# Kernel tuning notes

Hardware: AMD Instinct MI355X
Metric: run time of the kernel (lower is better)

The kernel has to match this reference:

```python
import jax, jax.numpy as jnp
import numpy as np

B, N, DIN, A = 64, 64, 64, 32
DOUT = 128          # obs_output_dim == obs_act_output_dim == 128 (required by module wiring)
OA_IN = DIN + A     # obs_act_input_dim = 96


def _w(key, shape):
    fan_in = shape[-1]
    return jax.random.normal(key, shape, jnp.float32) / jnp.sqrt(jnp.float32(fan_in))


def setup_inputs() -> dict:
    key = jax.random.key(0)
    ks = jax.random.split(key, 14)
    return {
        "states": jax.random.normal(ks[0], (B, N, DIN), jnp.float32),
        "policies": jax.random.uniform(ks[1], (B, N, A), jnp.float32),
        "actions": jax.random.uniform(ks[2], (B, N, A), jnp.float32),
        # state_embed_preproc: Linear(obs_input_dim, 128) + LeakyReLU
        "W_se_pre": _w(ks[3], (128, DIN)),
        "b_se_pre": jnp.zeros((128,), jnp.float32),
        # key/query layers (shared between both attention stages in forward)
        "W_key": _w(ks[4], (DOUT, 128)),
        "W_query": _w(ks[5], (DOUT, 128)),
        # state_embed: Linear(obs_output_dim, 128) + LeakyReLU
        "W_se": _w(ks[6], (128, DOUT)),
        "b_se": jnp.zeros((128,), jnp.float32),
        # state_act_pol_embed: Linear(obs_act_input_dim, 128) + LeakyReLU
        "W_sap": _w(ks[7], (128, OA_IN)),
        "b_sap": jnp.zeros((128,), jnp.float32),
        # attention_value_layer: Linear(128, obs_act_output_dim)
        "W_av": _w(ks[8], (DOUT, 128)),
        # final value head
        "W_f1": _w(ks[9], (64, DOUT)),
        "W_f2": _w(ks[10], (1, 64)),
    }


def reference(states, policies, actions, W_se_pre, b_se_pre, W_key, W_query,
              W_se, b_se, W_sap, b_sap, W_av, W_f1, W_f2):
    lrelu = jax.nn.leaky_relu  # negative_slope=0.01, matches torch default
    d_k = W_key.shape[0]
    inv_sqrt_dk = 1.0 / jnp.sqrt(jnp.asarray(d_k, states.dtype))

    # stage 1: self-attention over agents on raw-state embeddings
    e = lrelu(states @ W_se_pre.T + b_se_pre)                       # [B,N,128]
    q1 = e @ W_query.T
    k1 = e @ W_key.T
    w_pre = jax.nn.softmax(jnp.einsum('bid,bjd->bij', q1, k1) * inv_sqrt_dk, axis=-1)
    # NB: attention_value_layer_preproc output is overwritten in the original forward;
    # the effective value is weight_preproc @ states_embed_preproc.
    av_pre = jnp.einsum('bij,bjd->bid', w_pre, e)                   # [B,N,128]

    # stage 2: self-attention weights over agents on re-embedded states
    se = lrelu(av_pre @ W_se.T + b_se)                              # [B,N,128]
    q2 = se @ W_query.T
    k2 = se @ W_key.T
    w = jax.nn.softmax(jnp.einsum('bid,bjd->bij', q2, k2) * inv_sqrt_dk, axis=-1)

    # obs_actions_policies[b,j,k] = (state_k, policy_k) if j==k else (state_k, action_k)
    obs_act = jnp.concatenate([states, actions], axis=-1)           # [B,N,OA_IN]
    obs_pol = jnp.concatenate([states, policies], axis=-1)
    n = states.shape[1]
    eye = jnp.eye(n, dtype=states.dtype)[None, :, :, None]          # [1,N,N,1]
    oap = eye * obs_pol[:, None, :, :] + (1.0 - eye) * obs_act[:, None, :, :]  # [B,N,N,OA_IN]

    emb = lrelu(oap @ W_sap.T + b_sap)                              # [B,N,N,128]
    av = emb @ W_av.T                                               # [B,N,N,DOUT]

    # fused form of repeat->weight->sum: node[b,i,j,d] = sum_k w[b,i,k] * av[b,j,k,d]
    node = jnp.einsum('bik,bjkd->bijd', w, av)                      # [B,N,N,DOUT]

    value = lrelu(node @ W_f1.T) @ W_f2.T                           # [B,N,N,1]
    return value, w_pre, w
```

## Files before the change

kernel.cpp:

```cpp
#include <hip/hip_runtime.h>

#define DEVFN __device__ __forceinline__

constexpr int BNN = 64 * 64 * 64;
constexpr float SCALE = 0.08838834764831845f;
constexpr float NSLOPE = 0.01f;

constexpr int OFF_WPRET = 0;
constexpr int OFF_WQT   = 8192;
constexpr int OFF_M     = 24576;
constexpr int OFF_WSET  = 40960;
constexpr int OFF_WSAPT = 57344;
constexpr int OFF_WAVT  = 69632;
constexpr int OFF_WF1T  = 86016;
constexpr int OFF_E     = 98304;
constexpr int OFF_Q     = 622592;
constexpr int OFF_ET    = 1146880;
constexpr int OFF_SET   = 1671168;
constexpr int OFF_HA    = 2195456;
constexpr int OFF_HD    = 2719744;


DEVFN void st128(int tid, const float* __restrict__ src, float* __restrict__ Bs, int rows) {
  const int n4 = rows * 32;
  for (int idx = tid; idx < n4; idx += 512) {
    const int r = idx >> 5, c = idx & 31;
    *reinterpret_cast<float4*>(&Bs[r * 132 + c * 4]) =
        *reinterpret_cast<const float4*>(&src[r * 128 + c * 4]);
  }
}

DEVFN void st64x(int tid, const float* __restrict__ src, float* __restrict__ Bs) {
  for (int idx = tid; idx < 1024; idx += 512) {
    const int r = idx >> 4, c = idx & 15;
    *reinterpret_cast<float4*>(&Bs[r * 68 + c * 4]) =
        *reinterpret_cast<const float4*>(&src[r * 64 + c * 4]);
  }
}

DEVFN void wrT(int tid, const float* __restrict__ S, float* __restrict__ dst, int rq) {
  const int fr = tid >> 2, a4 = tid & 3;
  float t[4];
#pragma unroll
  for (int i = 0; i < 4; ++i) t[i] = S[(a4 * 4 + i) * 132 + fr];
  float4 v; v.x = t[0]; v.y = t[1]; v.z = t[2]; v.w = t[3];
  *reinterpret_cast<float4*>(&dst[fr * 64 + rq * 16 + a4 * 4]) = v;
}


DEVFN void g1(int tid, const float* __restrict__ A, int lda,
              const float* __restrict__ Bs, int K, float (&acc)[4]) {
  const int c0 = (tid & 31) * 4, rg = tid >> 5;
#pragma unroll 8
  for (int k = 0; k < K; ++k) {
    const float4 bv = *reinterpret_cast<const float4*>(&Bs[k * 132 + c0]);
    const float a = A[rg * lda + k];
    acc[0] += a * bv.x; acc[1] += a * bv.y; acc[2] += a * bv.z; acc[3] += a * bv.w;
  }
}

DEVFN void g2A(int tid, const float* __restrict__ A0, const float* __restrict__ A1,
               int lda, const float* __restrict__ Bs, int K,
               float (&a0)[4], float (&a1)[4]) {
  const int c0 = (tid & 31) * 4, rg = tid >> 5;
#pragma unroll 4
  for (int k = 0; k < K; ++k) {
    const float4 bv = *reinterpret_cast<const float4*>(&Bs[k * 132 + c0]);
    const float x = A0[rg * lda + k];
    const float y = A1[rg * lda + k];
    a0[0] += x * bv.x; a0[1] += x * bv.y; a0[2] += x * bv.z; a0[3] += x * bv.w;
    a1[0] += y * bv.x; a1[1] += y * bv.y; a1[2] += y * bv.z; a1[3] += y * bv.w;
  }
}

DEVFN void gH(int tid, const float* __restrict__ A, int lda,
              const float* __restrict__ Bs, int K, float (&acc)[2]) {
  const int c0 = (tid & 31) * 2, rg = tid >> 5;
#pragma unroll 8
  for (int k = 0; k < K; ++k) {
    const float2 bv = *reinterpret_cast<const float2*>(&Bs[k * 68 + c0]);
    const float a = A[rg * lda + k];
    acc[0] += a * bv.x; acc[1] += a * bv.y;
  }
}

DEVFN void gH2(int tid, const float* __restrict__ A0, const float* __restrict__ A1,
               int lda, const float* __restrict__ Bs, int K,
               float (&a0)[2], float (&a1)[2]) {
  const int c0 = (tid & 31) * 2, rg = tid >> 5;
#pragma unroll 4
  for (int k = 0; k < K; ++k) {
    const float2 bv = *reinterpret_cast<const float2*>(&Bs[k * 68 + c0]);
    const float x = A0[rg * lda + k];
    const float y = A1[rg * lda + k];
    a0[0] += x * bv.x; a0[1] += x * bv.y;
    a1[0] += y * bv.x; a1[1] += y * bv.y;
  }
}

template<bool ACT, bool HASB>
DEVFN void epi(int tid, const float (&acc)[4], float* __restrict__ O, int ldo,
               const float* __restrict__ bias) {
  const int c0 = (tid & 31) * 4, rg = tid >> 5;
  float t[4];
#pragma unroll
  for (int i = 0; i < 4; ++i) {
    float x = acc[i];
    if constexpr (HASB) x += bias[c0 + i];
    if constexpr (ACT) x = (x > 0.f) ? x : NSLOPE * x;
    t[i] = x;
  }
  float4 v; v.x = t[0]; v.y = t[1]; v.z = t[2]; v.w = t[3];
  *reinterpret_cast<float4*>(&O[rg * ldo + c0]) = v;
}


DEVFN void score_half(int tid, const float* __restrict__ Qs, int hoff,
                      const float* __restrict__ Ks, float (&acc)[2]) {
  const int j = tid & 63, iw = tid >> 6;
#pragma unroll 2
  for (int kt = 0; kt < 64; kt += 8) {
    float qv[2][8];
#pragma unroll
    for (int r = 0; r < 2; ++r) {
      *reinterpret_cast<float4*>(&qv[r][0]) =
          *reinterpret_cast<const float4*>(&Qs[(iw * 2 + r) * 132 + hoff + kt]);
      *reinterpret_cast<float4*>(&qv[r][4]) =
          *reinterpret_cast<const float4*>(&Qs[(iw * 2 + r) * 132 + hoff + kt + 4]);
    }
#pragma unroll
    for (int kk = 0; kk < 8; ++kk) {
      const float kv = Ks[(kt + kk) * 68 + j];
      acc[0] += qv[0][kk] * kv;
      acc[1] += qv[1][kk] * kv;
    }
  }
}

DEVFN void softmax_write(int tid, float (&acc)[2], float* __restrict__ Wp,
                         float* __restrict__ gout) {
  const int j = tid & 63, iw = tid >> 6;
#pragma unroll
  for (int r = 0; r < 2; ++r) {
    float v = acc[r] * SCALE;
    float m = v;
#pragma unroll
    for (int off = 32; off > 0; off >>= 1) m = fmaxf(m, __shfl_xor(m, off, 64));
    const float p = __expf(v - m);
    float s = p;
#pragma unroll
    for (int off = 32; off > 0; off >>= 1) s += __shfl_xor(s, off, 64);
    const float w = p / s;
    Wp[(iw * 2 + r) * 68 + j] = w;
    gout[(iw * 2 + r) * 64 + j] = w;
  }
}


__global__ void transpose_all(const float* __restrict__ Wpre, const float* __restrict__ Wq,
                              const float* __restrict__ Wse, const float* __restrict__ Wsap,
                              const float* __restrict__ Wav, const float* __restrict__ Wf1,
                              float* __restrict__ ws) {
  const int m = blockIdx.y;
  const float* src; int Cout, K, off;
  switch (m) {
    case 0: src = Wpre; Cout = 128; K = 64;  off = OFF_WPRET; break;
    case 1: src = Wq;   Cout = 128; K = 128; off = OFF_WQT;   break;
    case 2: src = Wse;  Cout = 128; K = 128; off = OFF_WSET;  break;
    case 3: src = Wsap; Cout = 128; K = 96;  off = OFF_WSAPT; break;
    case 4: src = Wav;  Cout = 128; K = 128; off = OFF_WAVT;  break;
    default: src = Wf1; Cout = 64;  K = 128; off = OFF_WF1T;  break;
  }
  const int idx = blockIdx.x * 256 + threadIdx.x;
  if (idx < Cout * K) {
    const int c = idx / K, k = idx - c * K;
    ws[off + k * Cout + c] = src[idx];
  }
}

__global__ __launch_bounds__(512) void make_M(const float* __restrict__ Wkey,
                                              float* __restrict__ ws) {
  __shared__ float As[16 * 132];
  __shared__ float Bs[64 * 132];
  const int tid = threadIdx.x;
  const int r0 = blockIdx.x * 16;
  {
    const int r = tid >> 5, c = tid & 31;
    *reinterpret_cast<float4*>(&As[r * 132 + c * 4]) =
        *reinterpret_cast<const float4*>(&ws[OFF_WQT + (r0 + r) * 128 + c * 4]);
  }
  const int c0 = (tid & 31) * 4, rg = tid >> 5;
  float acc[4] = {};
  for (int h = 0; h < 2; ++h) {
    __syncthreads();
    st128(tid, Wkey + h * 8192, Bs, 64);
    __syncthreads();
#pragma unroll 8
    for (int k = 0; k < 64; ++k) {
      const float4 bv = *reinterpret_cast<const float4*>(&Bs[k * 132 + c0]);
      const float a = As[rg * 132 + h * 64 + k];
      acc[0] += a * bv.x; acc[1] += a * bv.y; acc[2] += a * bv.z; acc[3] += a * bv.w;
    }
  }
  float4 v; v.x = acc[0]; v.y = acc[1]; v.z = acc[2]; v.w = acc[3];
  *reinterpret_cast<float4*>(&ws[OFF_M + (r0 + rg) * 128 + c0]) = v;
}

__global__ __launch_bounds__(512) void P1(const float* __restrict__ states,
                                          const float* __restrict__ policies,
                                          const float* __restrict__ actions,
                                          const float* __restrict__ b_sap,
                                          const float* __restrict__ b_se_pre,
                                          float* __restrict__ ws) {
  __shared__ float S[16 * 68];
  __shared__ float Aa[16 * 36], Ap[16 * 36];
  __shared__ float Ea[16 * 132];
  __shared__ float Ep[16 * 132], Dd[16 * 132], Er[16 * 132];
  __shared__ float Bs[64 * 132];
  const int tid = threadIdx.x;
  const int wid = ((blockIdx.x & 7) << 5) | (blockIdx.x >> 3);
  const int b = wid >> 2, rq = wid & 3;
  const int r0g = b * 64 + rq * 16;

  for (int idx = tid; idx < 1024; idx += 512) {
    const int r = idx >> 6, c = idx & 63;
    S[r * 68 + c] = states[(r0g + r) * 64 + c];
  }
  {
    const int r = tid >> 5, c = tid & 31;
    Aa[r * 36 + c] = actions[(r0g + r) * 32 + c];
    Ap[r * 36 + c] = policies[(r0g + r) * 32 + c];
  }
  st128(tid, ws + OFF_WSAPT, Bs, 64);
  __syncthreads();
  float cm[4] = {};
  g1(tid, S, 68, Bs, 64, cm);
  __syncthreads();
  st128(tid, ws + OFF_WSAPT + 8192, Bs, 32);
  __syncthreads();
  float aa[4] = {cm[0], cm[1], cm[2], cm[3]};
  float ap[4] = {cm[0], cm[1], cm[2], cm[3]};
  g2A(tid, Aa, Ap, 36, Bs, 32, aa, ap);
  epi<true, true>(tid, aa, Ea, 132, b_sap);
  epi<true, true>(tid, ap, Ep, 132, b_sap);
  __syncthreads();
  for (int idx = tid; idx < 2048; idx += 512) {
    const int r = idx >> 7, c = idx & 127;
    Ep[r * 132 + c] -= Ea[r * 132 + c];
  }
  __syncthreads();
  st128(tid, ws + OFF_WAVT, Bs, 64);
  __syncthreads();
  float av[4] = {}, dl[4] = {};
  g2A(tid, Ea, Ep, 132, Bs, 64, av, dl);
  __syncthreads();
  st128(tid, ws + OFF_WAVT + 8192, Bs, 64);
  __syncthreads();
  g2A(tid, Ea + 64, Ep + 64, 132, Bs, 64, av, dl);
  __syncthreads();
  epi<false, false>(tid, av, Ea, 132, nullptr);
  epi<false, false>(tid, dl, Dd, 132, nullptr);
  __syncthreads();
  st64x(tid, ws + OFF_WF1T, Bs);
  __syncthreads();
  float ah[2] = {}, aha[2] = {};
  gH2(tid, Dd, Ea, 132, Bs, 64, ah, aha);
  __syncthreads();
  st64x(tid, ws + OFF_WF1T + 4096, Bs);
  __syncthreads();
  gH2(tid, Dd + 64, Ea + 64, 132, Bs, 64, ah, aha);
  {
    const int c0 = (tid & 31) * 2, rg = tid >> 5;
    float2 vh; vh.x = ah[0]; vh.y = ah[1];
    float2 va; va.x = aha[0]; va.y = aha[1];
    *reinterpret_cast<float2*>(&ws[OFF_HD + (r0g + rg) * 64 + c0]) = vh;
    *reinterpret_cast<float2*>(&ws[OFF_HA + (r0g + rg) * 64 + c0]) = va;
  }
  __syncthreads();
  st128(tid, ws + OFF_WPRET, Bs, 64);
  __syncthreads();
  {
    float ae[4] = {};
    g1(tid, S, 68, Bs, 64, ae);
    const int c0 = (tid & 31) * 4, rg = tid >> 5;
    float t[4];
#pragma unroll
    for (int i = 0; i < 4; ++i) {
      float x = ae[i] + b_se_pre[c0 + i];
      t[i] = (x > 0.f) ? x : NSLOPE * x;
    }
    float4 v; v.x = t[0]; v.y = t[1]; v.z = t[2]; v.w = t[3];
    *reinterpret_cast<float4*>(&Er[rg * 132 + c0]) = v;
    *reinterpret_cast<float4*>(&ws[OFF_E + (r0g + rg) * 128 + c0]) = v;
  }
  __syncthreads();
  wrT(tid, Er, ws + OFF_ET + b * 8192, rq);
  st128(tid, ws + OFF_M, Bs, 64);
  __syncthreads();
  float af[4] = {};
  g1(tid, Er, 132, Bs, 64, af);
  __syncthreads();
  st128(tid, ws + OFF_M + 8192, Bs, 64);
  __syncthreads();
  g1(tid, Er + 64, 132, Bs, 64, af);
  epi<false, false>(tid, af, ws + OFF_Q + r0g * 128, 128, nullptr);
}

__global__ __launch_bounds__(512) void P3(const float* __restrict__ b_se,
                                          float* __restrict__ ws,
                                          float* __restrict__ out) {
  __shared__ float Qs[16 * 132];
  __shared__ float Bs[64 * 132];
  __shared__ float Wp[16 * 68], AV[16 * 132], SEr[16 * 132];
  const int tid = threadIdx.x;
  const int wid = ((blockIdx.x & 7) << 5) | (blockIdx.x >> 3);
  const int b = wid >> 2, rq = wid & 3;
  const int r0g = b * 64 + rq * 16;

  {
    const int r = tid >> 5, c = tid & 31;
    *reinterpret_cast<float4*>(&Qs[r * 132 + c * 4]) =
        *reinterpret_cast<const float4*>(&ws[OFF_Q + (r0g + r) * 128 + c * 4]);
  }
  st64x(tid, ws + OFF_ET + b * 8192, Bs);
  __syncthreads();
  float sc[2] = {};
  score_half(tid, Qs, 0, Bs, sc);
  __syncthreads();
  st64x(tid, ws + OFF_ET + b * 8192 + 4096, Bs);
  __syncthreads();
  score_half(tid, Qs, 64, Bs, sc);
  softmax_write(tid, sc, Wp, out + BNN + b * 4096 + rq * 1024);
  __syncthreads();
  st128(tid, ws + OFF_E + b * 8192, Bs, 64);
  __syncthreads();
  {
    float a[4] = {};
    g1(tid, Wp, 68, Bs, 64, a);
    epi<false, false>(tid, a, AV, 132, nullptr);
  }
  __syncthreads();
  st128(tid, ws + OFF_WSET, Bs, 64);
  __syncthreads();
  float as[4] = {};
  g1(tid, AV, 132, Bs, 64, as);
  __syncthreads();
  st128(tid, ws + OFF_WSET + 8192, Bs, 64);
  __syncthreads();
  g1(tid, AV + 64, 132, Bs, 64, as);
  {
    const int c0 = (tid & 31) * 4, rg = tid >> 5;
    float t[4];
#pragma unroll
    for (int i = 0; i < 4; ++i) {
      float x = as[i] + b_se[c0 + i];
      t[i] = (x > 0.f) ? x : NSLOPE * x;
    }
    float4 v; v.x = t[0]; v.y = t[1]; v.z = t[2]; v.w = t[3];
    *reinterpret_cast<float4*>(&SEr[rg * 132 + c0]) = v;
  }
  __syncthreads();
  wrT(tid, SEr, ws + OFF_SET + b * 8192, rq);
  st128(tid, ws + OFF_M, Bs, 64);
  __syncthreads();
  float af[4] = {};
  g1(tid, SEr, 132, Bs, 64, af);
  __syncthreads();
  st128(tid, ws + OFF_M + 8192, Bs, 64);
  __syncthreads();
  g1(tid, SEr + 64, 132, Bs, 64, af);
  epi<false, false>(tid, af, ws + OFF_Q + r0g * 128, 128, nullptr);
}

__global__ __launch_bounds__(512) void P4(const float* __restrict__ Wf2g,
                                          float* __restrict__ ws,
                                          float* __restrict__ out) {
  __shared__ float Qs[16 * 132];
  __shared__ float Bs[64 * 132];
  __shared__ float Wp[16 * 68], Hb[16 * 66];
  __shared__ float Hd[64 * 69];
  __shared__ float Wf2s[64];
  const int tid = threadIdx.x;
  const int wid = ((blockIdx.x & 7) << 5) | (blockIdx.x >> 3);
  const int b = wid >> 2, rq = wid & 3;
  const int r0g = b * 64 + rq * 16;

  for (int idx = tid; idx < 4096; idx += 512)
    Hd[(idx >> 6) * 69 + (idx & 63)] = ws[OFF_HD + b * 4096 + idx];
  if (tid < 64) Wf2s[tid] = Wf2g[tid];
  {
    const int r = tid >> 5, c = tid & 31;
    *reinterpret_cast<float4*>(&Qs[r * 132 + c * 4]) =
        *reinterpret_cast<const float4*>(&ws[OFF_Q + (r0g + r) * 128 + c * 4]);
  }
  st64x(tid, ws + OFF_SET + b * 8192, Bs);
  __syncthreads();
  float sc[2] = {};
  score_half(tid, Qs, 0, Bs, sc);
  __syncthreads();
  st64x(tid, ws + OFF_SET + b * 8192 + 4096, Bs);
  __syncthreads();
  score_half(tid, Qs, 64, Bs, sc);
  softmax_write(tid, sc, Wp, out + 2 * BNN + b * 4096 + rq * 1024);
  __syncthreads();
  st64x(tid, ws + OFF_HA + b * 4096, Bs);
  __syncthreads();
  float ah[2] = {};
  gH(tid, Wp, 68, Bs, 64, ah);
  {
    const int c0 = (tid & 31) * 2, rg = tid >> 5;
    float2 v; v.x = ah[0]; v.y = ah[1];
    *reinterpret_cast<float2*>(&Hb[rg * 66 + c0]) = v;
  }
  __syncthreads();
  const int j = tid & 63, iw = tid >> 6;
  float wv[2], a2[2] = {0.f, 0.f};
#pragma unroll
  for (int r = 0; r < 2; ++r) wv[r] = Wp[(iw * 2 + r) * 68 + j];
  for (int f = 0; f < 64; ++f) {
    const float hdv = Hd[j * 69 + f];
    const float wf = Wf2s[f];
#pragma unroll
    for (int r = 0; r < 2; ++r) {
      float t = Hb[(iw * 2 + r) * 66 + f] + wv[r] * hdv;
      t = (t > 0.f) ? t : NSLOPE * t;
      a2[r] += t * wf;
    }
  }
#pragma unroll
  for (int r = 0; r < 2; ++r)
    out[(r0g + iw * 2 + r) * 64 + j] = a2[r];
}

extern "C" void kernel_launch(void* const* d_in, const int* in_sizes, int n_in,
                              void* d_out, int out_size, void* d_ws, size_t ws_size,
                              hipStream_t stream) {
  const float* states   = (const float*)d_in[0];
  const float* policies = (const float*)d_in[1];
  const float* actions  = (const float*)d_in[2];
  const float* W_se_pre = (const float*)d_in[3];
  const float* b_se_pre = (const float*)d_in[4];
  const float* W_key    = (const float*)d_in[5];
  const float* W_query  = (const float*)d_in[6];
  const float* W_se     = (const float*)d_in[7];
  const float* b_se     = (const float*)d_in[8];
  const float* W_sap    = (const float*)d_in[9];
  const float* b_sap    = (const float*)d_in[10];
  const float* W_av     = (const float*)d_in[11];
  const float* W_f1     = (const float*)d_in[12];
  const float* W_f2     = (const float*)d_in[13];
  float* out = (float*)d_out;
  float* ws  = (float*)d_ws;

  transpose_all<<<dim3(64, 6), dim3(256), 0, stream>>>(
      W_se_pre, W_query, W_se, W_sap, W_av, W_f1, ws);
  make_M<<<dim3(8), dim3(512), 0, stream>>>(W_key, ws);
  P1<<<dim3(256), dim3(512), 0, stream>>>(states, policies, actions, b_sap, b_se_pre, ws);
  P3<<<dim3(256), dim3(512), 0, stream>>>(b_se, ws, out);
  P4<<<dim3(256), dim3(512), 0, stream>>>(W_f2, ws, out);
}
```

Before: 64.59 us.

## Fuse all stages into one persistent kernel with grid-wide barriers

Replaces the five separate launches (weight transpose, M precompute, P1, P3, P4) with a single 256-block kernel. Stages are separated by atomic-counter grid barriers, and a memset resets the counters. Per-block Q tiles now stay in shared memory across stages instead of round-tripping through global memory, and the score loops load the full 128-deep K tile at once. This cuts launch overhead and global traffic, but relies on all 256 blocks being co-resident and adds spin-wait barrier costs plus a memset launch.

Result: slower. 110.8 us (+71.5%).

```diff
diff --git a/kernel.cpp b/kernel.cpp
--- a/kernel.cpp
+++ b/kernel.cpp
@@ -7,18 +7,27 @@
 constexpr float NSLOPE = 0.01f;
 
 constexpr int OFF_WPRET = 0;
-constexpr int OFF_WQT   = 8192;
+constexpr int OFF_CNT   = 8192;
 constexpr int OFF_M     = 24576;
 constexpr int OFF_WSET  = 40960;
 constexpr int OFF_WSAPT = 57344;
 constexpr int OFF_WAVT  = 69632;
 constexpr int OFF_WF1T  = 86016;
 constexpr int OFF_E     = 98304;
-constexpr int OFF_Q     = 622592;
 constexpr int OFF_ET    = 1146880;
 constexpr int OFF_SET   = 1671168;
 constexpr int OFF_HA    = 2195456;
 constexpr int OFF_HD    = 2719744;
+
+constexpr int R_WP = 0;
+constexpr int R_AA = 1088;
+constexpr int R_AP = 1664;
+constexpr int R_QS = 2240;
+constexpr int R_EP = 4352;
+constexpr int R_DD = 6464;
+constexpr int R_ER = 8576;
+constexpr int R_BS = 10880;
+constexpr int LDS_TOT = 19584;
 
 
 DEVFN void st128(int tid, const float* __restrict__ src, float* __restrict__ Bs, int rows) {
@@ -30,8 +39,9 @@
   }
 }
 
-DEVFN void st64x(int tid, const float* __restrict__ src, float* __restrict__ Bs) {
-  for (int idx = tid; idx < 1024; idx += 512) {
+DEVFN void st64r(int tid, const float* __restrict__ src, float* __restrict__ Bs, int rows) {
+  const int n4 = rows * 16;
+  for (int idx = tid; idx < n4; idx += 512) {
     const int r = idx >> 4, c = idx & 15;
     *reinterpret_cast<float4*>(&Bs[r * 68 + c * 4]) =
         *reinterpret_cast<const float4*>(&src[r * 64 + c * 4]);
@@ -115,18 +125,18 @@
 }
 
 
-DEVFN void score_half(int tid, const float* __restrict__ Qs, int hoff,
+DEVFN void score_full(int tid, const float* __restrict__ Qs,
                       const float* __restrict__ Ks, float (&acc)[2]) {
   const int j = tid & 63, iw = tid >> 6;
 #pragma unroll 2
-  for (int kt = 0; kt < 64; kt += 8) {
+  for (int kt = 0; kt < 128; kt += 8) {
     float qv[2][8];
 #pragma unroll
     for (int r = 0; r < 2; ++r) {
       *reinterpret_cast<float4*>(&qv[r][0]) =
-          *reinterpret_cast<const float4*>(&Qs[(iw * 2 + r) * 132 + hoff + kt]);
+          *reinterpret_cast<const float4*>(&Qs[(iw * 2 + r) * 132 + kt]);
       *reinterpret_cast<float4*>(&qv[r][4]) =
-          *reinterpret_cast<const float4*>(&Qs[(iw * 2 + r) * 132 + hoff + kt + 4]);
+          *reinterpret_cast<const float4*>(&Qs[(iw * 2 + r) * 132 + kt + 4]);
     }
 #pragma unroll
     for (int kk = 0; kk < 8; ++kk) {
@@ -157,279 +167,274 @@
 }
 
 
-__global__ void transpose_all(const float* __restrict__ Wpre, const float* __restrict__ Wq,
-                              const float* __restrict__ Wse, const float* __restrict__ Wsap,
-                              const float* __restrict__ Wav, const float* __restrict__ Wf1,
-                              float* __restrict__ ws) {
-  const int m = blockIdx.y;
-  const float* src; int Cout, K, off;
-  switch (m) {
-    case 0: src = Wpre; Cout = 128; K = 64;  off = OFF_WPRET; break;
-    case 1: src = Wq;   Cout = 128; K = 128; off = OFF_WQT;   break;
-    case 2: src = Wse;  Cout = 128; K = 128; off = OFF_WSET;  break;
-    case 3: src = Wsap; Cout = 128; K = 96;  off = OFF_WSAPT; break;
-    case 4: src = Wav;  Cout = 128; K = 128; off = OFF_WAVT;  break;
-    default: src = Wf1; Cout = 64;  K = 128; off = OFF_WF1T;  break;
-  }
-  const int idx = blockIdx.x * 256 + threadIdx.x;
-  if (idx < Cout * K) {
-    const int c = idx / K, k = idx - c * K;
-    ws[off + k * Cout + c] = src[idx];
-  }
-}
-
-__global__ __launch_bounds__(512) void make_M(const float* __restrict__ Wkey,
-                                              float* __restrict__ ws) {
-  __shared__ float As[16 * 132];
-  __shared__ float Bs[64 * 132];
+DEVFN void gridbar(unsigned* __restrict__ cnt, int tid) {
+  __syncthreads();
+  if (tid == 0) {
+    __threadfence();
+    atomicAdd(cnt, 1u);
+    while (atomicAdd(cnt, 0u) < 256u) { __builtin_amdgcn_s_sleep(2); }
+    __threadfence();
+  }
+  __syncthreads();
+}
+
+
+__global__ __launch_bounds__(512) void FUSED(
+    const float* __restrict__ states, const float* __restrict__ policies,
+    const float* __restrict__ actions, const float* __restrict__ Wpre,
+    const float* __restrict__ bpre, const float* __restrict__ Wkey,
+    const float* __restrict__ Wq, const float* __restrict__ Wse,
+    const float* __restrict__ bse, const float* __restrict__ Wsap,
+    const float* __restrict__ bsap, const float* __restrict__ Wav,
+    const float* __restrict__ Wf1, const float* __restrict__ Wf2,
+    float* __restrict__ ws, float* __restrict__ out) {
+  __shared__ float L[LDS_TOT];
   const int tid = threadIdx.x;
-  const int r0 = blockIdx.x * 16;
-  {
-    const int r = tid >> 5, c = tid & 31;
-    *reinterpret_cast<float4*>(&As[r * 132 + c * 4]) =
-        *reinterpret_cast<const float4*>(&ws[OFF_WQT + (r0 + r) * 128 + c * 4]);
-  }
-  const int c0 = (tid & 31) * 4, rg = tid >> 5;
-  float acc[4] = {};
-  for (int h = 0; h < 2; ++h) {
-    __syncthreads();
-    st128(tid, Wkey + h * 8192, Bs, 64);
-    __syncthreads();
-#pragma unroll 8
-    for (int k = 0; k < 64; ++k) {
-      const float4 bv = *reinterpret_cast<const float4*>(&Bs[k * 132 + c0]);
-      const float a = As[rg * 132 + h * 64 + k];
-      acc[0] += a * bv.x; acc[1] += a * bv.y; acc[2] += a * bv.z; acc[3] += a * bv.w;
-    }
-  }
-  float4 v; v.x = acc[0]; v.y = acc[1]; v.z = acc[2]; v.w = acc[3];
-  *reinterpret_cast<float4*>(&ws[OFF_M + (r0 + rg) * 128 + c0]) = v;
-}
-
-__global__ __launch_bounds__(512) void P1(const float* __restrict__ states,
-                                          const float* __restrict__ policies,
-                                          const float* __restrict__ actions,
-                                          const float* __restrict__ b_sap,
-                                          const float* __restrict__ b_se_pre,
-                                          float* __restrict__ ws) {
-  __shared__ float S[16 * 68];
-  __shared__ float Aa[16 * 36], Ap[16 * 36];
-  __shared__ float Ea[16 * 132];
-  __shared__ float Ep[16 * 132], Dd[16 * 132], Er[16 * 132];
-  __shared__ float Bs[64 * 132];
-  const int tid = threadIdx.x;
-  const int wid = ((blockIdx.x & 7) << 5) | (blockIdx.x >> 3);
+  const int bid = blockIdx.x;
+  const int wid = ((bid & 7) << 5) | (bid >> 3);
   const int b = wid >> 2, rq = wid & 3;
   const int r0g = b * 64 + rq * 16;
-
-  for (int idx = tid; idx < 1024; idx += 512) {
-    const int r = idx >> 6, c = idx & 63;
-    S[r * 68 + c] = states[(r0g + r) * 64 + c];
-  }
+  unsigned* cnt = (unsigned*)(ws + OFF_CNT);
+
   {
-    const int r = tid >> 5, c = tid & 31;
-    Aa[r * 36 + c] = actions[(r0g + r) * 32 + c];
-    Ap[r * 36 + c] = policies[(r0g + r) * 32 + c];
-  }
-  st128(tid, ws + OFF_WSAPT, Bs, 64);
-  __syncthreads();
-  float cm[4] = {};
-  g1(tid, S, 68, Bs, 64, cm);
-  __syncthreads();
-  st128(tid, ws + OFF_WSAPT + 8192, Bs, 32);
-  __syncthreads();
-  float aa[4] = {cm[0], cm[1], cm[2], cm[3]};
-  float ap[4] = {cm[0], cm[1], cm[2], cm[3]};
-  g2A(tid, Aa, Ap, 36, Bs, 32, aa, ap);
-  epi<true, true>(tid, aa, Ea, 132, b_sap);
-  epi<true, true>(tid, ap, Ep, 132, b_sap);
-  __syncthreads();
-  for (int idx = tid; idx < 2048; idx += 512) {
-    const int r = idx >> 7, c = idx & 127;
-    Ep[r * 132 + c] -= Ea[r * 132 + c];
-  }
-  __syncthreads();
-  st128(tid, ws + OFF_WAVT, Bs, 64);
-  __syncthreads();
-  float av[4] = {}, dl[4] = {};
-  g2A(tid, Ea, Ep, 132, Bs, 64, av, dl);
-  __syncthreads();
-  st128(tid, ws + OFF_WAVT + 8192, Bs, 64);
-  __syncthreads();
-  g2A(tid, Ea + 64, Ep + 64, 132, Bs, 64, av, dl);
-  __syncthreads();
-  epi<false, false>(tid, av, Ea, 132, nullptr);
-  epi<false, false>(tid, dl, Dd, 132, nullptr);
-  __syncthreads();
-  st64x(tid, ws + OFF_WF1T, Bs);
-  __syncthreads();
-  float ah[2] = {}, aha[2] = {};
-  gH2(tid, Dd, Ea, 132, Bs, 64, ah, aha);
-  __syncthreads();
-  st64x(tid, ws + OFF_WF1T + 4096, Bs);
-  __syncthreads();
-  gH2(tid, Dd + 64, Ea + 64, 132, Bs, 64, ah, aha);
+    const int gt = bid * 512 + tid;
+    if (gt < 8192) {
+      const int c = gt >> 6, k = gt & 63;
+      ws[OFF_WPRET + k * 128 + c] = Wpre[gt];
+    } else if (gt < 24576) {
+      const int i = gt - 8192, c = i >> 7, k = i & 127;
+      ws[OFF_WSET + k * 128 + c] = Wse[i];
+    } else if (gt < 36864) {
+      const int i = gt - 24576, c = i / 96, k = i - c * 96;
+      ws[OFF_WSAPT + k * 128 + c] = Wsap[i];
+    } else if (gt < 53248) {
+      const int i = gt - 36864, c = i >> 7, k = i & 127;
+      ws[OFF_WAVT + k * 128 + c] = Wav[i];
+    } else if (gt < 61440) {
+      const int i = gt - 53248, c = i >> 7, k = i & 127;
+      ws[OFF_WF1T + k * 64 + c] = Wf1[i];
+    }
+  }
+  if (bid < 8) {
+    const int r0 = bid * 16;
+    float* As = L + R_QS;
+    float* Bs = L + R_BS;
+    for (int idx = tid; idx < 2048; idx += 512) {
+      const int r = idx & 15, o = idx >> 4;
+      As[r * 132 + o] = Wq[o * 128 + r0 + r];
+    }
+    const int c0 = (tid & 31) * 4, rg = tid >> 5;
+    float acc[4] = {};
+    for (int h = 0; h < 2; ++h) {
+      __syncthreads();
+      st128(tid, Wkey + h * 8192, Bs, 64);
+      __syncthreads();
+#pragma unroll 8
+      for (int k = 0; k < 64; ++k) {
+        const float4 bv = *reinterpret_cast<const float4*>(&Bs[k * 132 + c0]);
+        const float a = As[rg * 132 + h * 64 + k];
+        acc[0] += a * bv.x; acc[1] += a * bv.y; acc[2] += a * bv.z; acc[3] += a * bv.w;
+      }
+    }
+    float4 v; v.x = acc[0]; v.y = acc[1]; v.z = acc[2]; v.w = acc[3];
+    *reinterpret_cast<float4*>(&ws[OFF_M + (r0 + rg) * 128 + c0]) = v;
+  }
+  gridbar(cnt + 0, tid);
+
   {
-    const int c0 = (tid & 31) * 2, rg = tid >> 5;
-    float2 vh; vh.x = ah[0]; vh.y = ah[1];
-    float2 va; va.x = aha[0]; va.y = aha[1];
-    *reinterpret_cast<float2*>(&ws[OFF_HD + (r0g + rg) * 64 + c0]) = vh;
-    *reinterpret_cast<float2*>(&ws[OFF_HA + (r0g + rg) * 64 + c0]) = va;
-  }
-  __syncthreads();
-  st128(tid, ws + OFF_WPRET, Bs, 64);
-  __syncthreads();
+    float* S  = L + R_WP;
+    float* Aa = L + R_AA;
+    float* Ap = L + R_AP;
+    float* Ea = L + R_QS;
+    float* Ep = L + R_EP;
+    float* Dd = L + R_DD;
+    float* Er = L + R_ER;
+    float* Bs = L + R_BS;
+
+    for (int idx = tid; idx < 1024; idx += 512) {
+      const int r = idx >> 6, c = idx & 63;
+      S[r * 68 + c] = states[(r0g + r) * 64 + c];
+    }
+    {
+      const int r = tid >> 5, c = tid & 31;
+      Aa[r * 36 + c] = actions[(r0g + r) * 32 + c];
+      Ap[r * 36 + c] = policies[(r0g + r) * 32 + c];
+    }
+    st128(tid, ws + OFF_WSAPT, Bs, 64);
+    __syncthreads();
+    float cm[4] = {};
+    g1(tid, S, 68, Bs, 64, cm);
+    __syncthreads();
+    st128(tid, ws + OFF_WSAPT + 8192, Bs, 32);
+    __syncthreads();
+    float aa[4] = {cm[0], cm[1], cm[2], cm[3]};
+    float ap[4] = {cm[0], cm[1], cm[2], cm[3]};
+    g2A(tid, Aa, Ap, 36, Bs, 32, aa, ap);
+    epi<true, true>(tid, aa, Ea, 132, bsap);
+    epi<true, true>(tid, ap, Ep, 132, bsap);
+    __syncthreads();
+    for (int idx = tid; idx < 2048; idx += 512) {
+      const int r = idx >> 7, c = idx & 127;
+      Ep[r * 132 + c] -= Ea[r * 132 + c];
+    }
+    __syncthreads();
+    st128(tid, ws + OFF_WAVT, Bs, 64);
+    __syncthreads();
+    float av[4] = {}, dl[4] = {};
+    g2A(tid, Ea, Ep, 132, Bs, 64, av, dl);
+    __syncthreads();
+    st128(tid, ws + OFF_WAVT + 8192, Bs, 64);
+    __syncthreads();
+    g2A(tid, Ea + 64, Ep + 64, 132, Bs, 64, av, dl);
+    __syncthreads();
+    epi<false, false>(tid, av, Ea, 132, nullptr);
+    epi<false, false>(tid, dl, Dd, 132, nullptr);
+    __syncthreads();
+    st64r(tid, ws + OFF_WF1T, Bs, 64);
+    __syncthreads();
+    float ah[2] = {}, aha[2] = {};
+    gH2(tid, Dd, Ea, 132, Bs, 64, ah, aha);
+    __syncthreads();
+    st64r(tid, ws + OFF_WF1T + 4096, Bs, 64);
+    __syncthreads();
+    gH2(tid, Dd + 64, Ea + 64, 132, Bs, 64, ah, aha);
+    {
+      const int c0 = (tid & 31) * 2, rg = tid >> 5;
+      float2 vh; vh.x = ah[0]; vh.y = ah[1];
+      float2 va; va.x = aha[0]; va.y = aha[1];
+      *reinterpret_cast<float2*>(&ws[OFF_HD + (r0g + rg) * 64 + c0]) = vh;
+      *reinterpret_cast<float2*>(&ws[OFF_HA + (r0g + rg) * 64 + c0]) = va;
+    }
+    __syncthreads();
+    st128(tid, ws + OFF_WPRET, Bs, 64);
+    __syncthreads();
+    {
+      float ae[4] = {};
+      g1(tid, S, 68, Bs, 64, ae);
+      const int c0 = (tid & 31) * 4, rg = tid >> 5;
+      float t[4];
+#pragma unroll
+      for (int i = 0; i < 4; ++i) {
+        float x = ae[i] + bpre[c0 + i];
+        t[i] = (x > 0.f) ? x : NSLOPE * x;
+      }
+      float4 v; v.x = t[0]; v.y = t[1]; v.z = t[2]; v.w = t[3];
+      *reinterpret_cast<float4*>(&Er[rg * 132 + c0]) = v;
+      *reinterpret_cast<float4*>(&ws[OFF_E + (r0g + rg) * 128 + c0]) = v;
+    }
+    __syncthreads();
+    wrT(tid, Er, ws + OFF_ET + b * 8192, rq);
+    st128(tid, ws + OFF_M, Bs, 64);
+    __syncthreads();
+    float af[4] = {};
+    g1(tid, Er, 132, Bs, 64, af);
+    __syncthreads();
+    st128(tid, ws + OFF_M + 8192, Bs, 64);
+    __syncthreads();
+    g1(tid, Er + 64, 132, Bs, 64, af);
+    epi<false, false>(tid, af, L + R_QS, 132, nullptr);
+  }
+  gridbar(cnt + 1, tid);
+
   {
-    float ae[4] = {};
-    g1(tid, S, 68, Bs, 64, ae);
-    const int c0 = (tid & 31) * 4, rg = tid >> 5;
-    float t[4];
-#pragma unroll
-    for (int i = 0; i < 4; ++i) {
-      float x = ae[i] + b_se_pre[c0 + i];
-      t[i] = (x > 0.f) ? x : NSLOPE * x;
-    }
-    float4 v; v.x = t[0]; v.y = t[1]; v.z = t[2]; v.w = t[3];
-    *reinterpret_cast<float4*>(&Er[rg * 132 + c0]) = v;
-    *reinterpret_cast<float4*>(&ws[OFF_E + (r0g + rg) * 128 + c0]) = v;
-  }
-  __syncthreads();
-  wrT(tid, Er, ws + OFF_ET + b * 8192, rq);
-  st128(tid, ws + OFF_M, Bs, 64);
-  __syncthreads();
-  float af[4] = {};
-  g1(tid, Er, 132, Bs, 64, af);
-  __syncthreads();
-  st128(tid, ws + OFF_M + 8192, Bs, 64);
-  __syncthreads();
-  g1(tid, Er + 64, 132, Bs, 64, af);
-  epi<false, false>(tid, af, ws + OFF_Q + r0g * 128, 128, nullptr);
-}
-
-__global__ __launch_bounds__(512) void P3(const float* __restrict__ b_se,
-                                          float* __restrict__ ws,
-                                          float* __restrict__ out) {
-  __shared__ float Qs[16 * 132];
-  __shared__ float Bs[64 * 132];
-  __shared__ float Wp[16 * 68], AV[16 * 132], SEr[16 * 132];
-  const int tid = threadIdx.x;
-  const int wid = ((blockIdx.x & 7) << 5) | (blockIdx.x >> 3);
-  const int b = wid >> 2, rq = wid & 3;
-  const int r0g = b * 64 + rq * 16;
+    float* Qs  = L + R_QS;
+    float* Wp  = L + R_WP;
+    float* AV  = L + R_EP;
+    float* SEr = L + R_DD;
+    float* Bs  = L + R_BS;
+
+    st64r(tid, ws + OFF_ET + b * 8192, Bs, 128);
+    __syncthreads();
+    float sc[2] = {};
+    score_full(tid, Qs, Bs, sc);
+    softmax_write(tid, sc, Wp, out + BNN + b * 4096 + rq * 1024);
+    __syncthreads();
+    st128(tid, ws + OFF_E + b * 8192, Bs, 64);
+    __syncthreads();
+    {
+      float a[4] = {};
+      g1(tid, Wp, 68, Bs, 64, a);
+      epi<false, false>(tid, a, AV, 132, nullptr);
+    }
+    __syncthreads();
+    st128(tid, ws + OFF_WSET, Bs, 64);
+    __syncthreads();
+    float as[4] = {};
+    g1(tid, AV, 132, Bs, 64, as);
+    __syncthreads();
+    st128(tid, ws + OFF_WSET + 8192, Bs, 64);
+    __syncthreads();
+    g1(tid, AV + 64, 132, Bs, 64, as);
+    {
+      const int c0 = (tid & 31) * 4, rg = tid >> 5;
+      float t[4];
+#pragma unroll
+      for (int i = 0; i < 4; ++i) {
+        float x = as[i] + bse[c0 + i];
+        t[i] = (x > 0.f) ? x : NSLOPE * x;
+      }
+      float4 v; v.x = t[0]; v.y = t[1]; v.z = t[2]; v.w = t[3];
+      *reinterpret_cast<float4*>(&SEr[rg * 132 + c0]) = v;
+    }
+    __syncthreads();
+    wrT(tid, SEr, ws + OFF_SET + b * 8192, rq);
+    st128(tid, ws + OFF_M, Bs, 64);
+    __syncthreads();
+    float af[4] = {};
+    g1(tid, SEr, 132, Bs, 64, af);
+    __syncthreads();
+    st128(tid, ws + OFF_M + 8192, Bs, 64);
+    __syncthreads();
+    g1(tid, SEr + 64, 132, Bs, 64, af);
+    epi<false, false>(tid, af, Qs, 132, nullptr);
+  }
+  gridbar(cnt + 2, tid);
 
   {
-    const int r = tid >> 5, c = tid & 31;
-    *reinterpret_cast<float4*>(&Qs[r * 132 + c * 4]) =
-        *reinterpret_cast<const float4*>(&ws[OFF_Q + (r0g + r) * 128 + c * 4]);
-  }
-  st64x(tid, ws + OFF_ET + b * 8192, Bs);
-  __syncthreads();
-  float sc[2] = {};
-  score_half(tid, Qs, 0, Bs, sc);
-  __syncthreads();
-  st64x(tid, ws + OFF_ET + b * 8192 + 4096, Bs);
-  __syncthreads();
-  score_half(tid, Qs, 64, Bs, sc);
-  softmax_write(tid, sc, Wp, out + BNN + b * 4096 + rq * 1024);
-  __syncthreads();
-  st128(tid, ws + OFF_E + b * 8192, Bs, 64);
-  __syncthreads();
-  {
-    float a[4] = {};
-    g1(tid, Wp, 68, Bs, 64, a);
-    epi<false, false>(tid, a, AV, 132, nullptr);
-  }
-  __syncthreads();
-  st128(tid, ws + OFF_WSET, Bs, 64);
-  __syncthreads();
-  float as[4] = {};
-  g1(tid, AV, 132, Bs, 64, as);
-  __syncthreads();
-  st128(tid, ws + OFF_WSET + 8192, Bs, 64);
-  __syncthreads();
-  g1(tid, AV + 64, 132, Bs, 64, as);
-  {
-    const int c0 = (tid & 31) * 4, rg = tid >> 5;
-    float t[4];
-#pragma unroll
-    for (int i = 0; i < 4; ++i) {
-      float x = as[i] + b_se[c0 + i];
-      t[i] = (x > 0.f) ? x : NSLOPE * x;
-    }
-    float4 v; v.x = t[0]; v.y = t[1]; v.z = t[2]; v.w = t[3];
-    *reinterpret_cast<float4*>(&SEr[rg * 132 + c0]) = v;
-  }
-  __syncthreads();
-  wrT(tid, SEr, ws + OFF_SET + b * 8192, rq);
-  st128(tid, ws + OFF_M, Bs, 64);
-  __syncthreads();
-  float af[4] = {};
-  g1(tid, SEr, 132, Bs, 64, af);
-  __syncthreads();
-  st128(tid, ws + OFF_M + 8192, Bs, 64);
-  __syncthreads();
-  g1(tid, SEr + 64, 132, Bs, 64, af);
-  epi<false, false>(tid, af, ws + OFF_Q + r0g * 128, 128, nullptr);
-}
-
-__global__ __launch_bounds__(512) void P4(const float* __restrict__ Wf2g,
-                                          float* __restrict__ ws,
-                                          float* __restrict__ out) {
-  __shared__ float Qs[16 * 132];
-  __shared__ float Bs[64 * 132];
-  __shared__ float Wp[16 * 68], Hb[16 * 66];
-  __shared__ float Hd[64 * 69];
-  __shared__ float Wf2s[64];
-  const int tid = threadIdx.x;
-  const int wid = ((blockIdx.x & 7) << 5) | (blockIdx.x >> 3);
-  const int b = wid >> 2, rq = wid & 3;
-  const int r0g = b * 64 + rq * 16;
-
-  for (int idx = tid; idx < 4096; idx += 512)
-    Hd[(idx >> 6) * 69 + (idx & 63)] = ws[OFF_HD + b * 4096 + idx];
-  if (tid < 64) Wf2s[tid] = Wf2g[tid];
-  {
-    const int r = tid >> 5, c = tid & 31;
-    *reinterpret_cast<float4*>(&Qs[r * 132 + c * 4]) =
-        *reinterpret_cast<const float4*>(&ws[OFF_Q + (r0g + r) * 128 + c * 4]);
-  }
-  st64x(tid, ws + OFF_SET + b * 8192, Bs);
-  __syncthreads();
-  float sc[2] = {};
-  score_half(tid, Qs, 0, Bs, sc);
-  __syncthreads();
-  st64x(tid, ws + OFF_SET + b * 8192 + 4096, Bs);
-  __syncthreads();
-  score_half(tid, Qs, 64, Bs, sc);
-  softmax_write(tid, sc, Wp, out + 2 * BNN + b * 4096 + rq * 1024);
-  __syncthreads();
-  st64x(tid, ws + OFF_HA + b * 4096, Bs);
-  __syncthreads();
-  float ah[2] = {};
-  gH(tid, Wp, 68, Bs, 64, ah);
-  {
-    const int c0 = (tid & 31) * 2, rg = tid >> 5;
-    float2 v; v.x = ah[0]; v.y = ah[1];
-    *reinterpret_cast<float2*>(&Hb[rg * 66 + c0]) = v;
-  }
-  __syncthreads();
-  const int j = tid & 63, iw = tid >> 6;
-  float wv[2], a2[2] = {0.f, 0.f};
-#pragma unroll
-  for (int r = 0; r < 2; ++r) wv[r] = Wp[(iw * 2 + r) * 68 + j];
-  for (int f = 0; f < 64; ++f) {
-    const float hdv = Hd[j * 69 + f];
-    const float wf = Wf2s[f];
-#pragma unroll
-    for (int r = 0; r < 2; ++r) {
-      float t = Hb[(iw * 2 + r) * 66 + f] + wv[r] * hdv;
-      t = (t > 0.f) ? t : NSLOPE * t;
-      a2[r] += t * wf;
-    }
-  }
-#pragma unroll
-  for (int r = 0; r < 2; ++r)
-    out[(r0g + iw * 2 + r) * 64 + j] = a2[r];
+    float* Qs   = L + R_QS;
+    float* Wp   = L + R_WP;
+    float* Hb   = L + R_EP;
+    float* Wf2s = L + R_EP + 1056;
+    float* Hd   = L + R_DD;
+    float* Bs   = L + R_BS;
+
+    for (int idx = tid; idx < 4096; idx += 512)
+      Hd[(idx >> 6) * 69 + (idx & 63)] = ws[OFF_HD + b * 4096 + idx];
+    if (tid < 64) Wf2s[tid] = Wf2[tid];
+    st64r(tid, ws + OFF_SET + b * 8192, Bs, 128);
+    __syncthreads();
+    float sc[2] = {};
+    score_full(tid, Qs, Bs, sc);
+    softmax_write(tid, sc, Wp, out + 2 * BNN + b * 4096 + rq * 1024);
+    __syncthreads();
+    st64r(tid, ws + OFF_HA + b * 4096, Bs, 64);
+    __syncthreads();
+    float ah[2] = {};
+    gH(tid, Wp, 68, Bs, 64, ah);
+    {
+      const int c0 = (tid & 31) * 2, rg = tid >> 5;
+      float2 v; v.x = ah[0]; v.y = ah[1];
+      *reinterpret_cast<float2*>(&Hb[rg * 66 + c0]) = v;
+    }
+    __syncthreads();
+    const int j = tid & 63, iw = tid >> 6;
+    float wv[2], a2[2] = {0.f, 0.f};
+#pragma unroll
+    for (int r = 0; r < 2; ++r) wv[r] = Wp[(iw * 2 + r) * 68 + j];
+    for (int f = 0; f < 64; ++f) {
+      const float hdv = Hd[j * 69 + f];
+      const float wf = Wf2s[f];
+#pragma unroll
+      for (int r = 0; r < 2; ++r) {
+        float t = Hb[(iw * 2 + r) * 66 + f] + wv[r] * hdv;
+        t = (t > 0.f) ? t : NSLOPE * t;
+        a2[r] += t * wf;
+      }
+    }
+#pragma unroll
+    for (int r = 0; r < 2; ++r)
+      out[(r0g + iw * 2 + r) * 64 + j] = a2[r];
+  }
 }
 
 extern "C" void kernel_launch(void* const* d_in, const int* in_sizes, int n_in,
@@ -452,10 +457,8 @@
   float* out = (float*)d_out;
   float* ws  = (float*)d_ws;
 
-  transpose_all<<<dim3(64, 6), dim3(256), 0, stream>>>(
-      W_se_pre, W_query, W_se, W_sap, W_av, W_f1, ws);
-  make_M<<<dim3(8), dim3(512), 0, stream>>>(W_key, ws);
-  P1<<<dim3(256), dim3(512), 0, stream>>>(states, policies, actions, b_sap, b_se_pre, ws);
-  P3<<<dim3(256), dim3(512), 0, stream>>>(b_se, ws, out);
-  P4<<<dim3(256), dim3(512), 0, stream>>>(W_f2, ws, out);
-}
+  hipMemsetAsync(ws + OFF_CNT, 0, 16, stream);
+  FUSED<<<dim3(256), dim3(512), 0, stream>>>(
+      states, policies, actions, W_se_pre, b_se_pre, W_key, W_query, W_se, b_se,
+      W_sap, b_sap, W_av, W_f1, W_f2, ws, out);
+}
```
